# Optimization experiments

Measured on AMD Instinct MI355X. Metric: run time of the kernel, lower is better.

The kernel has to match this reference:

```python
import jax, jax.numpy as jnp
import numpy as np

B, N, D, H = 4, 2048, 256, 4
NT, ET = 5, 6
HEAD = D // H


def _linear_params(k, fan_in, fan_out):
    # torch nn.Linear default init: U(-1/sqrt(fan_in), 1/sqrt(fan_in)) for W and b
    bound = 1.0 / np.sqrt(fan_in)
    kw, kb = jax.random.split(k)
    W = jax.random.uniform(kw, (fan_in, fan_out), minval=-bound, maxval=bound, dtype=jnp.float32)
    b = jax.random.uniform(kb, (fan_out,), minval=-bound, maxval=bound, dtype=jnp.float32)
    return W, b


def setup_inputs() -> dict:
    key = jax.random.key(0)
    ks = jax.random.split(key, 10)
    Wq, bq = _linear_params(ks[0], D, D)
    Wk, bk = _linear_params(ks[1], D, D)
    Wv, bv = _linear_params(ks[2], D, D)
    Wo, bo = _linear_params(ks[3], D, D)
    return {
        "nodes": jax.random.normal(ks[4], (B, N, D), dtype=jnp.float32),
        "node_types": jax.random.randint(ks[5], (B, N), 0, NT, dtype=jnp.int32),
        "edge_types": jax.random.randint(ks[6], (B, N, N), 0, ET, dtype=jnp.int32),
        "adjacency": jax.random.randint(ks[7], (B, N, N), 0, 2).astype(jnp.float32),
        "node_type_embed": jax.random.normal(ks[8], (NT, D), dtype=jnp.float32),  # nn.Embedding ~ N(0,1)
        "edge_type_embed": jax.random.normal(ks[9], (ET, H), dtype=jnp.float32),
        "Wq": Wq, "bq": bq, "Wk": Wk, "bk": bk, "Wv": Wv, "bv": bv, "Wo": Wo, "bo": bo,
        "ln_g": jnp.ones((D,), jnp.float32),
        "ln_b": jnp.zeros((D,), jnp.float32),
    }


def reference(nodes, node_types, edge_types, adjacency, node_type_embed, edge_type_embed,
              Wq, bq, Wk, bk, Wv, bv, Wo, bo, ln_g, ln_b):
    # add node-type embeddings (residual below uses the typed nodes, as in the torch code)
    x = nodes + node_type_embed[node_types]                      # [B,N,D]

    def split_heads(t):
        return t.reshape(B, N, H, HEAD).transpose(0, 2, 1, 3)    # [B,H,N,HEAD]

    Q = split_heads(x @ Wq + bq)
    K = split_heads(x @ Wk + bk)
    V = split_heads(x @ Wv + bv)

    scores = jnp.einsum('bhnd,bhmd->bhnm', Q, K) / np.sqrt(HEAD).astype(np.float32)

    # edge-type bias: [B,N,N,H] -> [B,H,N,N]
    scores = scores + jnp.transpose(edge_type_embed[edge_types], (0, 3, 1, 2))

    # type-match soft mask: match -> +0.1, mismatch -> -0.05  (== tm*0.15 - 0.05)
    tm = (node_types[:, :, None] == node_types[:, None, :]).astype(jnp.float32)
    scores = scores + (tm * 0.15 - 0.05)[:, None]

    # adjacency hard mask
    scores = scores + ((1.0 - adjacency) * -1e9)[:, None]

    attn = jax.nn.softmax(scores, axis=-1)                        # [B,H,N,N]
    ctx = jnp.einsum('bhnm,bhmd->bhnd', attn, V)
    ctx = ctx.transpose(0, 2, 1, 3).reshape(B, N, D)

    out = ctx @ Wo + bo
    y = x + out
    mu = jnp.mean(y, axis=-1, keepdims=True)
    var = jnp.var(y, axis=-1, keepdims=True)
    y = (y - mu) * jax.lax.rsqrt(var + 1e-5) * ln_g + ln_b
    return y, attn
```

## Files before the change

kernel.cpp:

```cpp
#include <hip/hip_runtime.h>

#define Bsz 4
#define Nn 2048
#define Dd 256
#define Hh 4
#define HD 64
#define NTt 5
#define ETt 6
#define LOG2E 1.4426950408889634f
#define MSUB 24.0f
#define SCLQ 0.18033688011112042f

typedef float f32x4 __attribute__((ext_vector_type(4)));
typedef __bf16 bf16x8 __attribute__((ext_vector_type(8)));
typedef unsigned int u32x4 __attribute__((ext_vector_type(4)));
typedef unsigned short u16;
typedef unsigned char u8;
typedef unsigned int uint;

static __device__ __forceinline__ u16 f2bf(float f) {
  unsigned int u = __builtin_bit_cast(unsigned int, f);
  u = (u + 0x7fffu + ((u >> 16) & 1u)) >> 16;
  return (u16)u;
}

static __device__ __forceinline__ bf16x8 ld8(const u16* p) {
  return __builtin_bit_cast(bf16x8, *(const u32x4*)p);
}

static __device__ __forceinline__ void stage16(const void* g, void* l) {
  __builtin_amdgcn_global_load_lds(
      (const __attribute__((address_space(1))) uint*)g,
      (__attribute__((address_space(3))) uint*)l, 16, 0, 0);
}

#define MFMA16(a, b, c) __builtin_amdgcn_mfma_f32_16x16x32_bf16((a), (b), (c), 0, 0, 0)

#define OFF_X      0u
#define OFF_XBF    8388608u
#define OFF_WQKVT  12582912u
#define OFF_WOT    12976128u
#define OFF_BQKV   13107200u
#define OFF_Q      13110272u
#define OFF_K      17304576u
#define OFF_VT     25693184u
#define OFF_CTX    29887488u
#define OFF_CODES  34081792u

__global__ void pack_kernel(const float* Wq, const float* Wk, const float* Wv,
                            const float* Wo, const float* bq, const float* bk,
                            const float* bv, u16* wqkvT, u16* woT, float* bqkv) {
  int tid = blockIdx.x * 256 + threadIdx.x;
  if (tid < 196608) {
    int c = tid >> 8, k = tid & 255;
    int which = c >> 8, cc = c & 255;
    const float* W = (which == 0) ? Wq : ((which == 1) ? Wk : Wv);
    wqkvT[tid] = f2bf(W[k * 256 + cc]);
  } else if (tid < 262144) {
    int t2 = tid - 196608;
    int c = t2 >> 8, k = t2 & 255;
    woT[t2] = f2bf(Wo[k * 256 + c]);
  } else if (tid < 262912) {
    int c = tid - 262144;
    int which = c >> 8, cc = c & 255;
    bqkv[c] = (which == 0) ? bq[cc] : ((which == 1) ? bk[cc] : bv[cc]);
  }
}

__global__ void embed_kernel(const float* nodes, const int* node_types,
                             const float* nte, float* xf, u16* xbf) {
  int t = blockIdx.x * 256 + threadIdx.x;
  int flat = t * 4;
  int bn = flat >> 8, d0 = flat & 255;
  int nt = node_types[bn];
  float4 nv = *(const float4*)(nodes + flat);
  float4 ev = *(const float4*)(nte + nt * 256 + d0);
  float4 x4;
  x4.x = nv.x + ev.x; x4.y = nv.y + ev.y; x4.z = nv.z + ev.z; x4.w = nv.w + ev.w;
  *(float4*)(xf + flat) = x4;
  ushort4 xb;
  xb.x = f2bf(x4.x); xb.y = f2bf(x4.y); xb.z = f2bf(x4.z); xb.w = f2bf(x4.w);
  *(ushort4*)(xbf + flat) = xb;
}

__global__ __launch_bounds__(256) void maskpack_kernel(
    const int* node_types, const int* edge_types, const float* adjacency,
    u8* codes) {
  int t = blockIdx.x * 256 + threadIdx.x;
  int lane = t & 63;
  int kt = (t >> 6) & 31;
  int qt = (t >> 11) & 127;
  int b = t >> 18;
  int l15 = lane & 15, l4 = lane >> 4;
  const int* etb = edge_types + (size_t)b * Nn * Nn;
  const float* adjb = adjacency + (size_t)b * Nn * Nn;
  const int* ntb = node_types + b * Nn;
  int qrow = qt * 16 + l15;
  int ntq = ntb[qrow];
  const int* etr = etb + (size_t)qrow * Nn;
  const float* adr = adjb + (size_t)qrow * Nn;
  unsigned int wds[4];
#pragma unroll
  for (int ks = 0; ks < 4; ++ks) {
    int k0 = kt * 64 + ks * 16 + l4 * 4;
    int4 et4 = *(const int4*)(etr + k0);
    float4 a4 = *(const float4*)(adr + k0);
    int4 nt4 = *(const int4*)(ntb + k0);
    int e[4] = {et4.x, et4.y, et4.z, et4.w};
    int n[4] = {nt4.x, nt4.y, nt4.z, nt4.w};
    float a[4] = {a4.x, a4.y, a4.z, a4.w};
    unsigned int acc = 0;
#pragma unroll
    for (int j = 0; j < 4; ++j) {
      int code = e[j] + ((ntq == n[j]) ? 6 : 0) + ((a[j] != 0.0f) ? 12 : 0);
      acc |= (unsigned int)(code * 4) << (8 * j);
    }
    wds[ks] = acc;
  }
  u32x4 out = {wds[0], wds[1], wds[2], wds[3]};
  *(u32x4*)(codes + (size_t)t * 16) = out;
}

__global__ __launch_bounds__(256) void qkv_kernel(const u16* xbf, const u16* wqkvT,
                                                  const float* bqkv,
                                                  u16* Qb, u16* Kb, u16* Vtb) {
  int cb = blockIdx.x;
  int rb = blockIdx.y;
  int w = threadIdx.x >> 6, lane = threadIdx.x & 63;
  int l15 = lane & 15, l4 = lane >> 4;
  int row0 = rb * 64 + w * 16;
  int col0 = cb * 64;
  const u16* xr = xbf + (size_t)(row0 + l15) * 256;
  f32x4 acc[4];
#pragma unroll
  for (int i = 0; i < 4; ++i) acc[i] = (f32x4){0.f, 0.f, 0.f, 0.f};
#pragma unroll
  for (int kst = 0; kst < 8; ++kst) {
    int k0 = kst * 32 + l4 * 8;
    bf16x8 a = ld8(xr + k0);
#pragma unroll
    for (int cs = 0; cs < 4; ++cs) {
      int col = col0 + cs * 16 + l15;
      bf16x8 bw = ld8(wqkvT + (size_t)col * 256 + k0);
      acc[cs] = MFMA16(a, bw, acc[cs]);
    }
  }
#pragma unroll
  for (int cs = 0; cs < 4; ++cs) {
    int col = col0 + cs * 16 + l15;
    float bias = bqkv[col];
    int which = col >> 8, c = col & 255;
    int h = c >> 6, hd = c & 63;
    float scale = (which == 0) ? SCLQ : 1.0f;
#pragma unroll
    for (int j = 0; j < 4; ++j) {
      int row = row0 + l4 * 4 + j;
      int bb = row >> 11, n = row & 2047;
      u16 val = f2bf((acc[cs][j] + bias) * scale);
      if (which == 2)
        Vtb[((size_t)((bb * Hh + h) * HD + hd)) * Nn + n] = val;
      else if (which == 0)
        Qb[(size_t)(((bb * Hh + h) * Nn + n)) * HD + hd] = val;
      else
        Kb[(size_t)(((bb * Hh + h) * Nn + n)) * HD + hd] = val;
    }
  }
}

__global__ __launch_bounds__(256) void attn_kernel(
    const u16* Qb, const u16* Kb, const u16* Vtb, const u8* codes,
    const float* ee_g, float* attn_out, u16* ctx_ws) {
  __shared__ __align__(16) char kvb[4][2][8192];
  __shared__ __align__(16) char pls[4][2048];
  __shared__ float lsh[4][16];

  int bid0 = blockIdx.x;
  int bid = ((bid0 & 7) << 8) | (bid0 >> 3);
  int qt = bid & 127;
  int h = (bid >> 7) & 3;
  int b = bid >> 9;
  int w = threadIdx.x >> 6, lane = threadIdx.x & 63;
  int l15 = lane & 15, l4 = lane >> 4;
  int q0 = qt * 16;
  int bh = b * Hh + h;
  int wk0 = w * 512;

  float lutv = 0.f;
  {
    int ln = lane;
    int et = ln - 6 * (ln / 6);
    int tm = (ln / 6) & 1;
    int adj = ln / 12;
    if (ln < 24)
      lutv = (ee_g[et * Hh + h] + (tm ? 0.10f : -0.05f)) * LOG2E +
             (adj ? 0.f : -1.442695041e9f) - MSUB;
  }
  int lut_i = __float_as_int(lutv);

  const u16* Qp = Qb + (size_t)(bh * Nn + q0 + l15) * HD;
  bf16x8 bq0 = ld8(Qp + l4 * 8);
  bf16x8 bq1 = ld8(Qp + 32 + l4 * 8);

  const char* Kgw = (const char*)(Kb + (size_t)bh * Nn * HD) + (size_t)wk0 * 128;
  const char* Vg = (const char*)(Vtb + (size_t)bh * HD * Nn);
  const u32x4* cp = (const u32x4*)codes + ((size_t)(b * 128 + qt) * 32) * 64;

  int oS[8];
  const char* KgS[8];
  const char* VgS[8];
#pragma unroll
  for (int j = 0; j < 8; ++j) {
    int o = j * 1024 + lane * 16;
    oS[j] = o;
    int row = o >> 7;
    int sz = (o ^ ((row & 7) << 4)) & 127;
    KgS[j] = Kgw + (size_t)row * 128 + sz;
    VgS[j] = Vg + (size_t)row * (Nn * 2) + wk0 * 2 + sz;
  }
  char* myb0 = (char*)kvb[w][0];
  char* myb1 = (char*)kvb[w][1];

  int sw = (l15 & 7) << 4;
  int ra = (l15 * 128 + l4 * 16) ^ sw;
  char* pwave = (char*)pls[w];
  int pwbase = l15 * 128;

  uint p[8][8];
  float accl = 0.f;

#pragma unroll
  for (int j = 0; j < 8; ++j) stage16(KgS[j], myb0 + oS[j]);
  u32x4 cw = cp[(size_t)(w * 8) * 64 + lane];

#pragma unroll
  for (int i = 0; i < 8; ++i) {
    u32x4 cwn = cw;
    if (i < 7) {
      char* nb = (i & 1) ? myb0 : myb1;
#pragma unroll
      for (int j = 0; j < 8; ++j)
        stage16(KgS[j] + (size_t)(i + 1) * 8192, nb + oS[j]);
      cwn = cp[(size_t)(w * 8 + i + 1) * 64 + lane];
    }
    __builtin_amdgcn_sched_barrier(0);
    if (i < 7) asm volatile("s_waitcnt vmcnt(9) lgkmcnt(0)" ::: "memory");
    else       asm volatile("s_waitcnt vmcnt(0) lgkmcnt(0)" ::: "memory");
    __builtin_amdgcn_sched_barrier(0);
    const char* kcur = (i & 1) ? myb1 : myb0;
#pragma unroll
    for (int ks = 0; ks < 4; ++ks) {
      unsigned int cword = cw[ks];
      f32x4 acc;
#pragma unroll
      for (int j = 0; j < 4; ++j)
        acc[j] = __int_as_float(
            __builtin_amdgcn_ds_bpermute((cword >> (8 * j)) & 0xFF, lut_i));
      acc = MFMA16(ld8((const u16*)(kcur + ra + ks * 2048)), bq0, acc);
      acc = MFMA16(ld8((const u16*)(kcur + (ra ^ 64) + ks * 2048)), bq1, acc);
      float e0 = __builtin_amdgcn_exp2f(acc[0]);
      float e1 = __builtin_amdgcn_exp2f(acc[1]);
      float e2 = __builtin_amdgcn_exp2f(acc[2]);
      float e3 = __builtin_amdgcn_exp2f(acc[3]);
      accl += (e0 + e1) + (e2 + e3);
      asm("v_cvt_pk_bf16_f32 %0, %1, %2" : "=v"(p[i][ks * 2]) : "v"(e0), "v"(e1));
      asm("v_cvt_pk_bf16_f32 %0, %1, %2" : "=v"(p[i][ks * 2 + 1]) : "v"(e2), "v"(e3));
    }
    cw = cwn;
  }
  accl += __shfl_xor(accl, 16);
  accl += __shfl_xor(accl, 32);
  if (lane < 16) lsh[w][lane] = accl;
  __syncthreads();
  float tot = lsh[0][l15] + lsh[1][l15] + lsh[2][l15] + lsh[3][l15];
  bool zrow = (tot == 0.0f);
  float cscale = zrow ? (1.0f / 2048.0f) : (1.0f / tot);

  f32x4 ctx[4];
#pragma unroll
  for (int i = 0; i < 4; ++i) ctx[i] = (f32x4){0.f, 0.f, 0.f, 0.f};
  float* attb = attn_out + (size_t)bh * Nn * Nn + (size_t)(q0 + l15) * Nn + wk0;

#pragma unroll
  for (int j = 0; j < 8; ++j) stage16(VgS[j], myb0 + oS[j]);

#pragma unroll
  for (int i = 0; i < 8; ++i) {
    if (i < 7) {
      char* nb = (i & 1) ? myb0 : myb1;
#pragma unroll
      for (int j = 0; j < 8; ++j)
        stage16(VgS[j] + (size_t)(i + 1) * 128, nb + oS[j]);
    }
    __builtin_amdgcn_sched_barrier(0);
    if (i == 0)     asm volatile("s_waitcnt vmcnt(8) lgkmcnt(0)" ::: "memory");
    else if (i < 7) asm volatile("s_waitcnt vmcnt(12) lgkmcnt(0)" ::: "memory");
    else            asm volatile("s_waitcnt vmcnt(4) lgkmcnt(0)" ::: "memory");
    __builtin_amdgcn_sched_barrier(0);
    const char* vcur = (i & 1) ? myb1 : myb0;

    uint pp[8];
#pragma unroll
    for (int r = 0; r < 8; ++r) pp[r] = zrow ? 0x3F803F80u : p[i][r];
#pragma unroll
    for (int ks = 0; ks < 4; ++ks) {
      int2 wv = {(int)pp[ks * 2], (int)pp[ks * 2 + 1]};
      *(int2*)(pwave + pwbase + ((ks * 32 + l4 * 8) ^ sw)) = wv;
    }
#pragma unroll
    for (int ks = 0; ks < 4; ++ks) {
      uint u0 = pp[ks * 2], u1 = pp[ks * 2 + 1];
      f32x4 o;
      o[0] = __int_as_float((int)(u0 << 16)) * cscale;
      o[1] = __int_as_float((int)(u0 & 0xFFFF0000u)) * cscale;
      o[2] = __int_as_float((int)(u1 << 16)) * cscale;
      o[3] = __int_as_float((int)(u1 & 0xFFFF0000u)) * cscale;
      __builtin_nontemporal_store(o, (f32x4*)(attb + i * 64 + ks * 16 + l4 * 4));
    }
#pragma unroll
    for (int half = 0; half < 2; ++half) {
      bf16x8 pa = ld8((const u16*)(pwave + pwbase + ((half * 64 + l4 * 16) ^ sw)));
#pragma unroll
      for (int d = 0; d < 4; ++d) {
        bf16x8 v = ld8((const u16*)(vcur + d * 2048 + l15 * 128 +
                                    ((half * 64 + l4 * 16) ^ sw)));
        ctx[d] = MFMA16(pa, v, ctx[d]);
      }
    }
  }

  float csr[4];
#pragma unroll
  for (int j = 0; j < 4; ++j)
    csr[j] = __int_as_float(
        __builtin_amdgcn_ds_bpermute((l4 * 4 + j) * 4, __float_as_int(cscale)));
#pragma unroll
  for (int d = 0; d < 4; ++d)
#pragma unroll
    for (int j = 0; j < 4; ++j) ctx[d][j] *= csr[j];

  __syncthreads();
  float* creg = (float*)kvb;
  if (w > 0) {
    float* cs_ = creg + ((size_t)(w - 1) * 64 + lane) * 17;
#pragma unroll
    for (int d = 0; d < 4; ++d)
#pragma unroll
      for (int j = 0; j < 4; ++j) cs_[d * 4 + j] = ctx[d][j];
  }
  __syncthreads();
  if (w == 0) {
    float* c0 = creg + (size_t)lane * 17;
    float* c1 = creg + ((size_t)64 + lane) * 17;
    float* c2 = creg + ((size_t)128 + lane) * 17;
#pragma unroll
    for (int d = 0; d < 4; ++d) {
      int col = h * 64 + d * 16 + l15;
#pragma unroll
      for (int j = 0; j < 4; ++j) {
        float v = ctx[d][j] + c0[d * 4 + j] + c1[d * 4 + j] + c2[d * 4 + j];
        int qrow = q0 + l4 * 4 + j;
        ctx_ws[(size_t)(b * Nn + qrow) * Dd + col] = f2bf(v);
      }
    }
  }
}

__global__ __launch_bounds__(256) void outln_kernel(const u16* ctxb, const u16* woT,
                                                    const float* bo, const float* xf,
                                                    const float* ln_g, const float* ln_b,
                                                    float* yout) {
  __shared__ float ytile[32][257];
  __shared__ float muS[32], rvS[32];
  int bm0 = blockIdx.x * 32;
  int w = threadIdx.x >> 6, lane = threadIdx.x & 63;
  int l15 = lane & 15, l4 = lane >> 4;
  f32x4 acc[2][4];
#pragma unroll
  for (int q = 0; q < 2; ++q)
#pragma unroll
    for (int i = 0; i < 4; ++i) acc[q][i] = (f32x4){0.f, 0.f, 0.f, 0.f};
#pragma unroll
  for (int kst = 0; kst < 8; ++kst) {
    int k0 = kst * 32 + l4 * 8;
    bf16x8 a0 = ld8(ctxb + (size_t)(bm0 + l15) * 256 + k0);
    bf16x8 a1 = ld8(ctxb + (size_t)(bm0 + 16 + l15) * 256 + k0);
#pragma unroll
    for (int ds_ = 0; ds_ < 4; ++ds_) {
      bf16x8 bw = ld8(woT + (size_t)(w * 64 + ds_ * 16 + l15) * 256 + k0);
      acc[0][ds_] = MFMA16(a0, bw, acc[0][ds_]);
      acc[1][ds_] = MFMA16(a1, bw, acc[1][ds_]);
    }
  }
#pragma unroll
  for (int qs = 0; qs < 2; ++qs)
#pragma unroll
    for (int ds_ = 0; ds_ < 4; ++ds_) {
      int col = w * 64 + ds_ * 16 + l15;
      float bof = bo[col];
#pragma unroll
      for (int j = 0; j < 4; ++j) {
        int row = qs * 16 + l4 * 4 + j;
        ytile[row][col] = acc[qs][ds_][j] + bof + xf[(size_t)(bm0 + row) * 256 + col];
      }
    }
  __syncthreads();
  int row = threadIdx.x >> 3, seg = threadIdx.x & 7;
  float ps = 0.f, pq = 0.f;
#pragma unroll
  for (int c = 0; c < 32; ++c) {
    float v = ytile[row][seg * 32 + c];
    ps += v; pq += v * v;
  }
  ps += __shfl_xor(ps, 1); pq += __shfl_xor(pq, 1);
  ps += __shfl_xor(ps, 2); pq += __shfl_xor(pq, 2);
  ps += __shfl_xor(ps, 4); pq += __shfl_xor(pq, 4);
  if (seg == 0) {
    float mu = ps * (1.0f / 256.0f);
    muS[row] = mu;
    rvS[row] = rsqrtf(pq * (1.0f / 256.0f) - mu * mu + 1e-5f);
  }
  __syncthreads();
  float mu = muS[row], rv = rvS[row];
  float* yr = yout + (size_t)(bm0 + row) * 256;
#pragma unroll
  for (int c0 = 0; c0 < 32; c0 += 4) {
    int c = seg * 32 + c0;
    float4 o;
    o.x = (ytile[row][c + 0] - mu) * rv * ln_g[c + 0] + ln_b[c + 0];
    o.y = (ytile[row][c + 1] - mu) * rv * ln_g[c + 1] + ln_b[c + 1];
    o.z = (ytile[row][c + 2] - mu) * rv * ln_g[c + 2] + ln_b[c + 2];
    o.w = (ytile[row][c + 3] - mu) * rv * ln_g[c + 3] + ln_b[c + 3];
    *(float4*)(yr + c) = o;
  }
}

extern "C" void kernel_launch(void* const* d_in, const int* in_sizes, int n_in,
                              void* d_out, int out_size, void* d_ws, size_t ws_size,
                              hipStream_t stream) {
  const float* nodes = (const float*)d_in[0];
  const int* node_types = (const int*)d_in[1];
  const int* edge_types = (const int*)d_in[2];
  const float* adjacency = (const float*)d_in[3];
  const float* nte = (const float*)d_in[4];
  const float* ee = (const float*)d_in[5];
  const float* Wq = (const float*)d_in[6];
  const float* bq = (const float*)d_in[7];
  const float* Wk = (const float*)d_in[8];
  const float* bk = (const float*)d_in[9];
  const float* Wv = (const float*)d_in[10];
  const float* bv = (const float*)d_in[11];
  const float* Wo = (const float*)d_in[12];
  const float* bo = (const float*)d_in[13];
  const float* ln_g = (const float*)d_in[14];
  const float* ln_b = (const float*)d_in[15];

  float* y = (float*)d_out;
  float* attn = y + (size_t)Bsz * Nn * Dd;

  char* ws = (char*)d_ws;
  float* xf = (float*)(ws + OFF_X);
  u16* xbf = (u16*)(ws + OFF_XBF);
  u16* wqkvT = (u16*)(ws + OFF_WQKVT);
  u16* woT = (u16*)(ws + OFF_WOT);
  float* bqkv = (float*)(ws + OFF_BQKV);
  u16* Qb = (u16*)(ws + OFF_Q);
  u16* Kb = (u16*)(ws + OFF_K);
  u16* Vtb = (u16*)(ws + OFF_VT);
  u16* ctxb = (u16*)(ws + OFF_CTX);
  u8* codes = (u8*)(ws + OFF_CODES);

  pack_kernel<<<1027, 256, 0, stream>>>(Wq, Wk, Wv, Wo, bq, bk, bv, wqkvT, woT, bqkv);
  embed_kernel<<<2048, 256, 0, stream>>>(nodes, node_types, nte, xf, xbf);
  maskpack_kernel<<<4096, 256, 0, stream>>>(node_types, edge_types, adjacency, codes);
  qkv_kernel<<<dim3(12, 128), 256, 0, stream>>>(xbf, wqkvT, bqkv, Qb, Kb, Vtb);
  attn_kernel<<<2048, 256, 0, stream>>>(Qb, Kb, Vtb, codes, ee, attn, ctxb);
  outln_kernel<<<256, 256, 0, stream>>>(ctxb, woT, bo, xf, ln_g, ln_b, y);
}
```

Measured before the change: 185.2 us.

## Fuse PV accumulation into the QK/exp loop with deferred normalization

The P·V MFMA accumulation moves into the same per-tile loop that computes QK scores and exponentials. Each wave now uses one LDS buffer for K and one for V instead of double-buffering K and then V across two separate passes. Normalization by the row sum is applied to the context only after the loop, and the attention-matrix stores remain a separate pass that applies a scale and bias. The aim is to remove the second full pass and its staging latency, at the cost of less load/compute overlap from single buffering. Rows whose sum is zero now get a zero context instead of the mean of V, which changes edge-case behaviour.

Measured after the change: 202.7 us. 1.09x slower.

```diff
diff --git a/kernel.cpp b/kernel.cpp
--- a/kernel.cpp
+++ b/kernel.cpp
@@ -217,8 +217,8 @@
     KgS[j] = Kgw + (size_t)row * 128 + sz;
     VgS[j] = Vg + (size_t)row * (Nn * 2) + wk0 * 2 + sz;
   }
-  char* myb0 = (char*)kvb[w][0];
-  char* myb1 = (char*)kvb[w][1];
+  char* kbuf = (char*)kvb[w][0];
+  char* vbuf = (char*)kvb[w][1];
 
   int sw = (l15 & 7) << 4;
   int ra = (l15 * 128 + l4 * 16) ^ sw;
@@ -227,26 +227,29 @@
 
   uint p[8][8];
   float accl = 0.f;
-
-#pragma unroll
-  for (int j = 0; j < 8; ++j) stage16(KgS[j], myb0 + oS[j]);
+  f32x4 ctx[4];
+#pragma unroll
+  for (int i = 0; i < 4; ++i) ctx[i] = (f32x4){0.f, 0.f, 0.f, 0.f};
+
+  asm volatile("s_waitcnt vmcnt(0)" ::: "memory");
+  __builtin_amdgcn_sched_barrier(0);
   u32x4 cw = cp[(size_t)(w * 8) * 64 + lane];
+#pragma unroll
+  for (int j = 0; j < 8; ++j) stage16(KgS[j], kbuf + oS[j]);
+  __builtin_amdgcn_sched_barrier(0);
 
 #pragma unroll
   for (int i = 0; i < 8; ++i) {
+#pragma unroll
+    for (int j = 0; j < 8; ++j)
+      stage16(VgS[j] + (size_t)i * 128, vbuf + oS[j]);
     u32x4 cwn = cw;
-    if (i < 7) {
-      char* nb = (i & 1) ? myb0 : myb1;
-#pragma unroll
-      for (int j = 0; j < 8; ++j)
-        stage16(KgS[j] + (size_t)(i + 1) * 8192, nb + oS[j]);
-      cwn = cp[(size_t)(w * 8 + i + 1) * 64 + lane];
-    }
+    if (i < 7) cwn = cp[(size_t)(w * 8 + i + 1) * 64 + lane];
     __builtin_amdgcn_sched_barrier(0);
     if (i < 7) asm volatile("s_waitcnt vmcnt(9) lgkmcnt(0)" ::: "memory");
-    else       asm volatile("s_waitcnt vmcnt(0) lgkmcnt(0)" ::: "memory");
-    __builtin_amdgcn_sched_barrier(0);
-    const char* kcur = (i & 1) ? myb1 : myb0;
+    else       asm volatile("s_waitcnt vmcnt(8) lgkmcnt(0)" ::: "memory");
+    __builtin_amdgcn_sched_barrier(0);
+
 #pragma unroll
     for (int ks = 0; ks < 4; ++ks) {
       unsigned int cword = cw[ks];
@@ -255,8 +258,8 @@
       for (int j = 0; j < 4; ++j)
         acc[j] = __int_as_float(
             __builtin_amdgcn_ds_bpermute((cword >> (8 * j)) & 0xFF, lut_i));
-      acc = MFMA16(ld8((const u16*)(kcur + ra + ks * 2048)), bq0, acc);
-      acc = MFMA16(ld8((const u16*)(kcur + (ra ^ 64) + ks * 2048)), bq1, acc);
+      acc = MFMA16(ld8((const u16*)(kbuf + ra + ks * 2048)), bq0, acc);
+      acc = MFMA16(ld8((const u16*)(kbuf + (ra ^ 64) + ks * 2048)), bq1, acc);
       float e0 = __builtin_amdgcn_exp2f(acc[0]);
       float e1 = __builtin_amdgcn_exp2f(acc[1]);
       float e2 = __builtin_amdgcn_exp2f(acc[2]);
@@ -265,69 +268,62 @@
       asm("v_cvt_pk_bf16_f32 %0, %1, %2" : "=v"(p[i][ks * 2]) : "v"(e0), "v"(e1));
       asm("v_cvt_pk_bf16_f32 %0, %1, %2" : "=v"(p[i][ks * 2 + 1]) : "v"(e2), "v"(e3));
     }
+    __builtin_amdgcn_sched_barrier(0);
+    asm volatile("s_waitcnt lgkmcnt(0)" ::: "memory");
+    __builtin_amdgcn_sched_barrier(0);
+    if (i < 7) {
+#pragma unroll
+      for (int j = 0; j < 8; ++j)
+        stage16(KgS[j] + (size_t)(i + 1) * 8192, kbuf + oS[j]);
+    }
+    __builtin_amdgcn_sched_barrier(0);
+    if (i < 7) asm volatile("s_waitcnt vmcnt(9) lgkmcnt(0)" ::: "memory");
+    else       asm volatile("s_waitcnt vmcnt(0) lgkmcnt(0)" ::: "memory");
+    __builtin_amdgcn_sched_barrier(0);
+
+#pragma unroll
+    for (int ks = 0; ks < 4; ++ks) {
+      int2 wv = {(int)p[i][ks * 2], (int)p[i][ks * 2 + 1]};
+      *(int2*)(pwave + pwbase + ((ks * 32 + l4 * 8) ^ sw)) = wv;
+    }
+#pragma unroll
+    for (int half = 0; half < 2; ++half) {
+      bf16x8 pa = ld8((const u16*)(pwave + pwbase + ((half * 64 + l4 * 16) ^ sw)));
+#pragma unroll
+      for (int d = 0; d < 4; ++d) {
+        bf16x8 v = ld8((const u16*)(vbuf + d * 2048 + l15 * 128 +
+                                    ((half * 64 + l4 * 16) ^ sw)));
+        ctx[d] = MFMA16(pa, v, ctx[d]);
+      }
+    }
     cw = cwn;
   }
+
   accl += __shfl_xor(accl, 16);
   accl += __shfl_xor(accl, 32);
   if (lane < 16) lsh[w][lane] = accl;
   __syncthreads();
   float tot = lsh[0][l15] + lsh[1][l15] + lsh[2][l15] + lsh[3][l15];
   bool zrow = (tot == 0.0f);
-  float cscale = zrow ? (1.0f / 2048.0f) : (1.0f / tot);
-
-  f32x4 ctx[4];
-#pragma unroll
-  for (int i = 0; i < 4; ++i) ctx[i] = (f32x4){0.f, 0.f, 0.f, 0.f};
+  float pscale = zrow ? 0.0f : 1.0f / tot;
+  float pbias = zrow ? (1.0f / 2048.0f) : 0.0f;
+
   float* attb = attn_out + (size_t)bh * Nn * Nn + (size_t)(q0 + l15) * Nn + wk0;
-
-#pragma unroll
-  for (int j = 0; j < 8; ++j) stage16(VgS[j], myb0 + oS[j]);
-
 #pragma unroll
   for (int i = 0; i < 8; ++i) {
-    if (i < 7) {
-      char* nb = (i & 1) ? myb0 : myb1;
-#pragma unroll
-      for (int j = 0; j < 8; ++j)
-        stage16(VgS[j] + (size_t)(i + 1) * 128, nb + oS[j]);
-    }
-    __builtin_amdgcn_sched_barrier(0);
-    if (i == 0)     asm volatile("s_waitcnt vmcnt(8) lgkmcnt(0)" ::: "memory");
-    else if (i < 7) asm volatile("s_waitcnt vmcnt(12) lgkmcnt(0)" ::: "memory");
-    else            asm volatile("s_waitcnt vmcnt(4) lgkmcnt(0)" ::: "memory");
-    __builtin_amdgcn_sched_barrier(0);
-    const char* vcur = (i & 1) ? myb1 : myb0;
-
-    uint pp[8];
-#pragma unroll
-    for (int r = 0; r < 8; ++r) pp[r] = zrow ? 0x3F803F80u : p[i][r];
 #pragma unroll
     for (int ks = 0; ks < 4; ++ks) {
-      int2 wv = {(int)pp[ks * 2], (int)pp[ks * 2 + 1]};
-      *(int2*)(pwave + pwbase + ((ks * 32 + l4 * 8) ^ sw)) = wv;
-    }
-#pragma unroll
-    for (int ks = 0; ks < 4; ++ks) {
-      uint u0 = pp[ks * 2], u1 = pp[ks * 2 + 1];
+      uint u0 = p[i][ks * 2], u1 = p[i][ks * 2 + 1];
       f32x4 o;
-      o[0] = __int_as_float((int)(u0 << 16)) * cscale;
-      o[1] = __int_as_float((int)(u0 & 0xFFFF0000u)) * cscale;
-      o[2] = __int_as_float((int)(u1 << 16)) * cscale;
-      o[3] = __int_as_float((int)(u1 & 0xFFFF0000u)) * cscale;
+      o[0] = __int_as_float((int)(u0 << 16)) * pscale + pbias;
+      o[1] = __int_as_float((int)(u0 & 0xFFFF0000u)) * pscale + pbias;
+      o[2] = __int_as_float((int)(u1 << 16)) * pscale + pbias;
+      o[3] = __int_as_float((int)(u1 & 0xFFFF0000u)) * pscale + pbias;
       __builtin_nontemporal_store(o, (f32x4*)(attb + i * 64 + ks * 16 + l4 * 4));
     }
-#pragma unroll
-    for (int half = 0; half < 2; ++half) {
-      bf16x8 pa = ld8((const u16*)(pwave + pwbase + ((half * 64 + l4 * 16) ^ sw)));
-#pragma unroll
-      for (int d = 0; d < 4; ++d) {
-        bf16x8 v = ld8((const u16*)(vcur + d * 2048 + l15 * 128 +
-                                    ((half * 64 + l4 * 16) ^ sw)));
-        ctx[d] = MFMA16(pa, v, ctx[d]);
-      }
-    }
-  }
-
+  }
+
+  float cscale = pscale + pbias;
   float csr[4];
 #pragma unroll
   for (int j = 0; j < 4; ++j)
```

## Coalesce maskpack reads via LDS staging of 16-row code tiles

Applied to the files above, without the earlier changes.

The mask-packing kernel now assigns one block per 16-row query tile. Its threads read edge_types and adjacency in fully contiguous row order, pack the byte codes into padded shared memory, then write them back out in the MFMA-fragment order the attention kernel expects. The old mapping had each lane read 16-byte pieces scattered across 16 rows, which gave poorly coalesced access to the large 64 MB inputs. The cost is 33 KB of LDS per block and a grid of only 512 blocks, which may limit memory-level parallelism.

Result: no change. 184.5 us (-0.4%).

```diff
diff --git a/kernel.cpp b/kernel.cpp
--- a/kernel.cpp
+++ b/kernel.cpp
@@ -86,39 +86,50 @@
 __global__ __launch_bounds__(256) void maskpack_kernel(
     const int* node_types, const int* edge_types, const float* adjacency,
     u8* codes) {
-  int t = blockIdx.x * 256 + threadIdx.x;
-  int lane = t & 63;
-  int kt = (t >> 6) & 31;
-  int qt = (t >> 11) & 127;
-  int b = t >> 18;
-  int l15 = lane & 15, l4 = lane >> 4;
-  const int* etb = edge_types + (size_t)b * Nn * Nn;
-  const float* adjb = adjacency + (size_t)b * Nn * Nn;
+  __shared__ uint lw[16 * 516 + 4];
+  int blk = blockIdx.x;
+  int qt = blk & 127;
+  int b = blk >> 7;
+  int t = threadIdx.x;
   const int* ntb = node_types + b * Nn;
-  int qrow = qt * 16 + l15;
-  int ntq = ntb[qrow];
-  const int* etr = etb + (size_t)qrow * Nn;
-  const float* adr = adjb + (size_t)qrow * Nn;
-  unsigned int wds[4];
-#pragma unroll
-  for (int ks = 0; ks < 4; ++ks) {
-    int k0 = kt * 64 + ks * 16 + l4 * 4;
-    int4 et4 = *(const int4*)(etr + k0);
-    float4 a4 = *(const float4*)(adr + k0);
+  const int* etb = edge_types + (size_t)b * Nn * Nn + (size_t)qt * 16 * Nn;
+  const float* adjb = adjacency + (size_t)b * Nn * Nn + (size_t)qt * 16 * Nn;
+
+#pragma unroll 4
+  for (int a = 0; a < 32; ++a) {
+    int idx = a * 256 + t;
+    int row = idx >> 9;
+    int k4 = idx & 511;
+    int k0 = k4 * 4;
+    int ntq = ntb[qt * 16 + row];
+    int4 et4 = *(const int4*)(etb + (size_t)row * Nn + k0);
+    float4 a4 = *(const float4*)(adjb + (size_t)row * Nn + k0);
     int4 nt4 = *(const int4*)(ntb + k0);
     int e[4] = {et4.x, et4.y, et4.z, et4.w};
     int n[4] = {nt4.x, nt4.y, nt4.z, nt4.w};
-    float a[4] = {a4.x, a4.y, a4.z, a4.w};
-    unsigned int acc = 0;
+    float av[4] = {a4.x, a4.y, a4.z, a4.w};
+    uint word = 0;
 #pragma unroll
     for (int j = 0; j < 4; ++j) {
-      int code = e[j] + ((ntq == n[j]) ? 6 : 0) + ((a[j] != 0.0f) ? 12 : 0);
-      acc |= (unsigned int)(code * 4) << (8 * j);
-    }
-    wds[ks] = acc;
-  }
-  u32x4 out = {wds[0], wds[1], wds[2], wds[3]};
-  *(u32x4*)(codes + (size_t)t * 16) = out;
+      int code = e[j] + ((ntq == n[j]) ? 6 : 0) + ((av[j] != 0.0f) ? 12 : 0);
+      word |= (uint)(code * 4) << (8 * j);
+    }
+    lw[row * 516 + k4] = word;
+  }
+  __syncthreads();
+
+  u8* rec = codes + (size_t)(b * 128 + qt) * 32768;
+#pragma unroll
+  for (int c = 0; c < 8; ++c) {
+    int W = (c * 256 + t) * 4;
+    int kt = W >> 8;
+    int rem = W & 255;
+    int l4 = rem >> 6;
+    int l15 = (rem >> 2) & 15;
+    int base = l15 * 516 + kt * 16 + l4;
+    u32x4 o = {lw[base], lw[base + 4], lw[base + 8], lw[base + 12]};
+    *(u32x4*)(rec + (size_t)W * 4) = o;
+  }
 }
 
 __global__ __launch_bounds__(256) void qkv_kernel(const u16* xbf, const u16* wqkvT,
@@ -471,7 +482,7 @@
 
   pack_kernel<<<1027, 256, 0, stream>>>(Wq, Wk, Wv, Wo, bq, bk, bv, wqkvT, woT, bqkv);
   embed_kernel<<<2048, 256, 0, stream>>>(nodes, node_types, nte, xf, xbf);
-  maskpack_kernel<<<4096, 256, 0, stream>>>(node_types, edge_types, adjacency, codes);
+  maskpack_kernel<<<512, 256, 0, stream>>>(node_types, edge_types, adjacency, codes);
   qkv_kernel<<<dim3(12, 128), 256, 0, stream>>>(xbf, wqkvT, bqkv, Qb, Kb, Vtb);
   attn_kernel<<<2048, 256, 0, stream>>>(Qb, Kb, Vtb, codes, ee, attn, ctxb);
   outln_kernel<<<256, 256, 0, stream>>>(ctxb, woT, bo, xf, ln_g, ln_b, y);
```
